# Kernel optimization log

Hardware: AMD Instinct MI355X
Metric: run time of the kernel (lower is better)

The kernel has to match this reference:

```python
import jax, jax.numpy as jnp
import numpy as np

K_ATTRS = 16  # fixed number of attribute clusters (torch.unique made static for jit)
NEG_INF = jnp.float32(-1e9)


def setup_inputs() -> dict:
    key = jax.random.key(0)
    ks = jax.random.split(key, 20)
    B, T, V, D, H = 4096, 200, 100000, 64, 64
    M0, M1 = 256, 128
    FC_IN = D + D + H + D  # 256
    s = 0.02
    f32 = jnp.float32
    inp = {
        "item_id": jax.random.randint(ks[0], (B,), 0, V),
        "hist_item_ids": jax.random.randint(ks[1], (B, T), 0, V),
        "hist_item_attributes": jax.random.randint(ks[2], (B, T), 0, K_ATTRS),
        "emb_table": s * jax.random.normal(ks[3], (V, D), dtype=f32),
        "au_W1": s * jax.random.normal(ks[4], (4 * D, H), dtype=f32),
        "au_b1": jnp.zeros((H,), f32),
        "au_W2": s * jax.random.normal(ks[5], (H, 1), dtype=f32),
        "au_b2": jnp.zeros((1,), f32),
        "gru_Wx": s * jax.random.normal(ks[6], (D, 3 * H), dtype=f32),
        "gru_Wh": s * jax.random.normal(ks[7], (H, 3 * H), dtype=f32),
        "gru_b": jnp.zeros((3 * H,), f32),
        "fc_W0": s * jax.random.normal(ks[8], (FC_IN, M0), dtype=f32),
        "fc_b0": jnp.zeros((M0,), f32),
        "fc_W1": s * jax.random.normal(ks[9], (M0, M1), dtype=f32),
        "fc_b1": jnp.zeros((M1,), f32),
        "final_W": s * jax.random.normal(ks[10], (M1, 1), dtype=f32),
        "final_b": jnp.zeros((1,), f32),
    }
    return inp


def reference(item_id, hist_item_ids, hist_item_attributes, emb_table,
              au_W1, au_b1, au_W2, au_b2, gru_Wx, gru_Wh, gru_b,
              fc_W0, fc_b0, fc_W1, fc_b1, final_W, final_b):
    item = emb_table[item_id]            # [B,D]
    hist = emb_table[hist_item_ids]      # [B,T,D]
    B = item.shape[0]
    H = gru_Wh.shape[0]

    # --- DIEN: GRU over history, final hidden state ---
    xp = hist @ gru_Wx + gru_b           # [B,T,3H]

    def step(h, x):
        gz, gr, gn = jnp.split(h @ gru_Wh, 3, axis=-1)
        xz, xr, xn = jnp.split(x, 3, axis=-1)
        z = jax.nn.sigmoid(xz + gz)
        r = jax.nn.sigmoid(xr + gr)
        n = jnp.tanh(xn + r * gn)
        return (1.0 - z) * n + z * h, None

    h0 = jnp.zeros((B, H), hist.dtype)
    interest_evolution, _ = jax.lax.scan(step, h0, jnp.swapaxes(xp, 0, 1))  # [B,H]

    # --- DIN-style activation unit: score each key against the target item ---
    def act_unit(q, keys):  # q:[B,D], keys:[B,N,D] -> [B,N,1]
        qe = jnp.broadcast_to(q[:, None, :], keys.shape)
        feat = jnp.concatenate([keys, qe, keys - qe, keys * qe], axis=-1)
        hid = jax.nn.relu(feat @ au_W1 + au_b1)
        return hid @ au_W2 + au_b2

    w1 = act_unit(item, hist)                    # [B,T,1]
    user_interest_l1 = jnp.sum(w1 * hist, axis=1)  # [B,D]

    # --- attribute_group: per-attribute masked softmax + weighted sum ---
    mask = hist_item_attributes[..., None] == jnp.arange(K_ATTRS)  # [B,T,K]
    logits = jnp.where(mask, w1, NEG_INF)        # [B,T,K]
    probs = jax.nn.softmax(logits, axis=1) * mask
    cluster = jnp.einsum('btk,btd->bkd', probs, hist)  # [B,K,D]

    w2 = act_unit(item, cluster)                 # [B,K,1]
    user_interest_l2 = jnp.sum(w2 * cluster, axis=1)  # [B,D]

    combined = jnp.concatenate(
        [user_interest_l1, user_interest_l2, interest_evolution, item], axis=1)
    x = jax.nn.relu(combined @ fc_W0 + fc_b0)
    x = jax.nn.relu(x @ fc_W1 + fc_b1)
    out = x @ final_W + final_b                  # [B,1]
    return jax.nn.sigmoid(out[:, 0])             # [B]
```

## Files before the change

kernel.cpp:

```cpp
#include <hip/hip_runtime.h>
#include <hip/hip_bf16.h>

#define B_   4096
#define T_   200
#define KA   16

#define OFF_BG  0
#define OFF_WQ  4096
#define OFF_QP  (OFF_BG  + B_*T_)
#define OFF_UI1 (OFF_QP  + B_*64)
#define OFF_UI2 (OFF_UI1 + B_*64)
#define OFF_HF  (OFF_UI2 + B_*64)
#define OFF_CL  (OFF_HF  + B_*64)

typedef __attribute__((ext_vector_type(8))) short bf16x8;
typedef __attribute__((ext_vector_type(4))) float f32x4;

__device__ __forceinline__ float sigmoidf_(float x) {
  return 1.f / (1.f + __expf(-x));
}
__device__ __forceinline__ float sigf(float x) {
  return __builtin_amdgcn_rcpf(1.f + __builtin_amdgcn_exp2f(-1.44269504f * x));
}
__device__ __forceinline__ float tanhfast(float y) {
  return 1.f - 2.f * __builtin_amdgcn_rcpf(1.f + __builtin_amdgcn_exp2f(2.88539008f * y));
}
__device__ __forceinline__ short f2bf(float x) {
  unsigned u = __float_as_uint(x);
  unsigned r = (u + 0x7fffu + ((u >> 16) & 1u)) >> 16;
  return (short)r;
}
__device__ __forceinline__ unsigned cvtpk(float lo, float hi) {
  unsigned r;
  asm("v_cvt_pk_bf16_f32 %0, %1, %2" : "=v"(r) : "v"(lo), "v"(hi));
  return r;
}
union BF8 { bf16x8 v; unsigned u[4]; };

__device__ __forceinline__ bf16x8 pack8(float4 f0, float4 f1) {
  BF8 a;
  a.u[0] = cvtpk(f0.x, f0.y);
  a.u[1] = cvtpk(f0.z, f0.w);
  a.u[2] = cvtpk(f1.x, f1.y);
  a.u[3] = cvtpk(f1.z, f1.w);
  return a.v;
}
__device__ __forceinline__ bf16x8 pack8m(float4 f0, float4 f1,
                                         float4 q0, float4 q1) {
  BF8 a;
  a.u[0] = cvtpk(f0.x*q0.x, f0.y*q0.y);
  a.u[1] = cvtpk(f0.z*q0.z, f0.w*q0.w);
  a.u[2] = cvtpk(f1.x*q1.x, f1.y*q1.y);
  a.u[3] = cvtpk(f1.z*q1.z, f1.w*q1.w);
  return a.v;
}


__global__ __launch_bounds__(256) void k_prep(
    const float* __restrict__ auW1, short* __restrict__ bg,
    float* __restrict__ wq)
{
  const int i = blockIdx.x*256 + threadIdx.x;
  if (i < 8192) {
    const int k = i >> 6, col = i & 63;
    float v;
    if (k < 64) v = auW1[k*64 + col] + auW1[2*4096 + k*64 + col];
    else        v = auW1[3*4096 + (k-64)*64 + col];
    bg[((k >> 5)*4 + ((k >> 3) & 3))*512 + col*8 + (k & 7)] = f2bf(v);
  } else if (i < 12288) {
    const int j = i - 8192;
    wq[j] = auW1[(64 + (j >> 6))*64 + (j & 63)]
          - auW1[(128 + (j >> 6))*64 + (j & 63)];
  }
}

__global__ __launch_bounds__(256) void k_act1(
    const int* __restrict__ item_id, const int* __restrict__ hist_ids,
    const int* __restrict__ attrs,
    const float* __restrict__ emb, const float* __restrict__ aub1,
    const float* __restrict__ auW2, const float* __restrict__ aub2,
    const short* __restrict__ bg_in, const float* __restrict__ wq_in,
    float* __restrict__ qp_out, float* __restrict__ ui1_out,
    float* __restrict__ cluster_out)
{
  __shared__ __align__(16) char sPool[16384];
  __shared__ float sW1[208];
  __shared__ float sP[200];
  __shared__ float sM[KA], sE[KA];
  __shared__ float sItem[64], sQp[64];
  __shared__ float sQpP[4][64];
  __shared__ float sUi[4][64];
  __shared__ int   sIds[200], sAttr[200];

  short* sB2 = (short*)sPool;
  float (*sAcc)[KA][64] = (float (*)[KA][64])sPool;

  const int b = blockIdx.x;
  const int tid = threadIdx.x;
  const int wave = tid >> 6, lane = tid & 63;
  const int g = lane >> 4;
  const int c15 = lane & 15;
  const int itrow = item_id[b];

  for (int i = tid; i < 4096; i += 256)
    ((unsigned*)sB2)[i] = ((const unsigned*)bg_in)[i];
  if (tid < 64) sItem[tid] = emb[(size_t)itrow*64 + tid];
  if (tid < T_) {
    sIds[tid]  = hist_ids[(size_t)b*T_ + tid];
    sAttr[tid] = attrs[(size_t)b*T_ + tid];
  }
  __syncthreads();

  {
    const int j = tid & 63, iq = tid >> 6;
    float acc = 0.f;
    #pragma unroll
    for (int ii = 0; ii < 16; ++ii) {
      const int i = iq*16 + ii;
      acc += sItem[i] * wq_in[i*64 + j];
    }
    sQpP[iq][j] = acc;
  }
  __syncthreads();
  if (tid < 64) {
    float q = aub1[tid] + sQpP[0][tid] + sQpP[1][tid] + sQpP[2][tid] + sQpP[3][tid];
    sQp[tid] = q;
    qp_out[(size_t)b*64 + tid] = q;
  }
  __syncthreads();

  const float4* itemp = (const float4*)(emb + (size_t)itrow*64);
  float4 q0 = itemp[g*2],     q1 = itemp[g*2 + 1];
  float4 q2 = itemp[8 + g*2], q3 = itemp[8 + g*2 + 1];

  bf16x8 bfr[4][4];
  #pragma unroll
  for (int kk = 0; kk < 4; ++kk) {
    #pragma unroll
    for (int n = 0; n < 4; ++n)
      bfr[kk][n] = *(const bf16x8*)&sB2[(kk*4 + g)*512 + (n*16 + c15)*8];
  }
  float w2v[4], qpv[4];
  #pragma unroll
  for (int n = 0; n < 4; ++n) {
    w2v[n] = auW2[n*16 + c15];
    qpv[n] = sQp[n*16 + c15];
  }
  const float b2v = aub2[0];
  __syncthreads();

  for (int i = tid; i < 4*KA*64; i += 256) ((float*)sAcc)[i] = 0.f;

  {
    float4 c0, c1, c2, c3;
    {
      const int t = wave*16 + c15;
      const int tc = (t < T_) ? t : (T_ - 1);
      const float4* kp = (const float4*)(emb + (size_t)sIds[tc]*64);
      c0 = kp[g*2];     c1 = kp[g*2 + 1];
      c2 = kp[8 + g*2]; c3 = kp[8 + g*2 + 1];
    }
    for (int tt = wave; tt < 13; tt += 4) {
      float4 n0{0,0,0,0}, n1{0,0,0,0}, n2{0,0,0,0}, n3{0,0,0,0};
      const int ttn = tt + 4;
      if (ttn < 13) {
        const int t = ttn*16 + c15;
        const int tc = (t < T_) ? t : (T_ - 1);
        const float4* kp = (const float4*)(emb + (size_t)sIds[tc]*64);
        n0 = kp[g*2];     n1 = kp[g*2 + 1];
        n2 = kp[8 + g*2]; n3 = kp[8 + g*2 + 1];
      }

      bf16x8 a0 = pack8(c0, c1);
      bf16x8 a1 = pack8(c2, c3);
      bf16x8 a2 = pack8m(c0, c1, q0, q1);
      bf16x8 a3 = pack8m(c2, c3, q2, q3);

      f32x4 acc[4];
      #pragma unroll
      for (int n = 0; n < 4; ++n) acc[n] = f32x4{qpv[n], qpv[n], qpv[n], qpv[n]};
      #pragma unroll
      for (int n = 0; n < 4; ++n) {
        acc[n] = __builtin_amdgcn_mfma_f32_16x16x32_bf16(a0, bfr[0][n], acc[n], 0, 0, 0);
        acc[n] = __builtin_amdgcn_mfma_f32_16x16x32_bf16(a1, bfr[1][n], acc[n], 0, 0, 0);
        acc[n] = __builtin_amdgcn_mfma_f32_16x16x32_bf16(a2, bfr[2][n], acc[n], 0, 0, 0);
        acc[n] = __builtin_amdgcn_mfma_f32_16x16x32_bf16(a3, bfr[3][n], acc[n], 0, 0, 0);
      }
      float ws[4] = {0.f, 0.f, 0.f, 0.f};
      #pragma unroll
      for (int n = 0; n < 4; ++n) {
        #pragma unroll
        for (int r = 0; r < 4; ++r)
          ws[r] += fmaxf(acc[n][r], 0.f) * w2v[n];
      }
      #pragma unroll
      for (int r = 0; r < 4; ++r) {
        ws[r] += __shfl_xor(ws[r], 1);
        ws[r] += __shfl_xor(ws[r], 2);
        ws[r] += __shfl_xor(ws[r], 4);
        ws[r] += __shfl_xor(ws[r], 8);
        ws[r] += b2v;
      }
      if (c15 == 0) {
        #pragma unroll
        for (int r = 0; r < 4; ++r) {
          const int trow = tt*16 + g*4 + r;
          if (trow < T_) sW1[trow] = ws[r];
        }
      }
      c0 = n0; c1 = n1; c2 = n2; c3 = n3;
    }
  }
  __syncthreads();

  for (int k = wave; k < KA; k += 4) {
    float m = -1e9f;
    for (int tt4 = 0; tt4 < 4; ++tt4) {
      int t = tt4*64 + lane;
      if (t < T_ && sAttr[t] == k) m = fmaxf(m, sW1[t]);
    }
    #pragma unroll
    for (int off = 32; off > 0; off >>= 1) m = fmaxf(m, __shfl_xor(m, off));
    float e = 0.f;
    for (int tt4 = 0; tt4 < 4; ++tt4) {
      int t = tt4*64 + lane;
      if (t < T_ && sAttr[t] == k) e += __expf(sW1[t] - m);
    }
    #pragma unroll
    for (int off = 32; off > 0; off >>= 1) e += __shfl_xor(e, off);
    if (lane == 0) { sM[k] = m; sE[k] = e; }
  }
  __syncthreads();
  if (tid < T_) {
    int k = sAttr[tid];
    float e = sE[k];
    sP[tid] = (e > 0.f) ? __expf(sW1[tid] - sM[k]) * __builtin_amdgcn_rcpf(e) : 0.f;
  }
  __syncthreads();

  {
    float uiacc = 0.f;
    #define LDV(tt) (((tt) < T_) ? emb[(size_t)sIds[tt]*64 + lane] : 0.f)
    float v0 = LDV(wave), v1 = LDV(wave + 4), v2 = LDV(wave + 8), v3 = LDV(wave + 12);
    for (int t = wave; t < T_; t += 16) {
      float n0 = LDV(t + 16), n1 = LDV(t + 20), n2 = LDV(t + 24), n3 = LDV(t + 28);
      {
        const int tt = t;
        if (tt < T_) { sAcc[wave][sAttr[tt]][lane] += sP[tt] * v0; uiacc += sW1[tt] * v0; }
      }
      {
        const int tt = t + 4;
        if (tt < T_) { sAcc[wave][sAttr[tt]][lane] += sP[tt] * v1; uiacc += sW1[tt] * v1; }
      }
      {
        const int tt = t + 8;
        if (tt < T_) { sAcc[wave][sAttr[tt]][lane] += sP[tt] * v2; uiacc += sW1[tt] * v2; }
      }
      {
        const int tt = t + 12;
        if (tt < T_) { sAcc[wave][sAttr[tt]][lane] += sP[tt] * v3; uiacc += sW1[tt] * v3; }
      }
      v0 = n0; v1 = n1; v2 = n2; v3 = n3;
    }
    #undef LDV
    sUi[wave][lane] = uiacc;
  }
  __syncthreads();

  for (int i = tid; i < KA*64; i += 256) {
    cluster_out[(size_t)b*(KA*64) + i] =
        sAcc[0][0][i] + sAcc[1][0][i] + sAcc[2][0][i] + sAcc[3][0][i];
  }
  if (tid < 64) {
    ui1_out[(size_t)b*64 + tid] =
        sUi[0][tid] + sUi[1][tid] + sUi[2][tid] + sUi[3][tid];
  }
}

#define GRU_ROWS 16
__global__ __launch_bounds__(512) void k_gru(
    const int* __restrict__ hist_ids, const float* __restrict__ emb,
    const float* __restrict__ Wx, const float* __restrict__ Wh,
    const float* __restrict__ gb, float* __restrict__ hfin_out)
{
  __shared__ short sH[2][16*64];
  __shared__ short sX[4][16*64];
  __shared__ int   sIds[16*200];

  const int tid  = threadIdx.x;
  const int w    = tid >> 6;
  const int lane = tid & 63;
  const int g    = lane >> 4;
  const int c15  = lane & 15;
  const int b0   = blockIdx.x * GRU_ROWS;

  for (int i = tid; i < 16*200; i += 512) {
    const int r = i / 200, t = i - r*200;
    sIds[i] = hist_ids[(size_t)(b0 + r)*T_ + t];
  }
  for (int i = tid; i < 16*64; i += 512) sH[0][i] = 0;
  __syncthreads();

  if (w >= 4) {
    const int stane = (w - 4)*64 + lane;
    const int srow  = stane >> 4;
    const int scol  = (stane & 15) * 4;
    const int sidx  = srow*64 + (((scol >> 3) ^ (srow & 7))*8) + (scol & 7);
    const int* idrow = &sIds[srow*200];
    #pragma unroll
    for (int p = 0; p < 2; ++p) {
      const float4 f = *(const float4*)(emb + (size_t)idrow[p]*64 + scol);
      uint2 u; u.x = cvtpk(f.x, f.y); u.y = cvtpk(f.z, f.w);
      *(uint2*)&sX[p][sidx] = u;
    }
    __syncthreads();
    for (int t = 0; t < T_; ++t) {
      const int t2 = (t + 2 < T_) ? (t + 2) : (T_ - 1);
      const float4 f = *(const float4*)(emb + (size_t)idrow[t2]*64 + scol);
      uint2 u; u.x = cvtpk(f.x, f.y); u.y = cvtpk(f.z, f.w);
      *(uint2*)&sX[(t + 2) & 3][sidx] = u;
      __syncthreads();
    }
  } else {
    bf16x8 bx[3][2], bh[3][2];
    #pragma unroll
    for (int l = 0; l < 3; ++l) {
      const int jb = (l*4 + w)*16 + c15;
      #pragma unroll
      for (int kk = 0; kk < 2; ++kk) {
        bf16x8 vx, vh;
        #pragma unroll
        for (int e = 0; e < 8; ++e) {
          const int krow = kk*32 + g*8 + e;
          vx[e] = f2bf(Wx[(size_t)krow*192 + jb]);
          vh[e] = f2bf(Wh[(size_t)krow*192 + jb]);
        }
        bx[l][kk] = vx; bh[l][kk] = vh;
      }
    }
    float bias[3];
    #pragma unroll
    for (int l = 0; l < 3; ++l) bias[l] = gb[l*64 + w*16 + c15];

    const int rs = c15 & 7;
    const int ridx0 = c15*64 + ((g    ) ^ rs)*8;
    const int ridx1 = c15*64 + ((g + 4) ^ rs)*8;
    int widx[4];
    {
      const int unit = w*2 + (c15 >> 3);
      #pragma unroll
      for (int r = 0; r < 4; ++r) {
        const int row = g*4 + r;
        widx[r] = row*64 + ((unit ^ (row & 7))*8) + (c15 & 7);
      }
    }
    float hold[4] = {0.f, 0.f, 0.f, 0.f};
    __syncthreads();

    #pragma unroll 2
    for (int t = 0; t < T_; ++t) {
      const short* hbuf = sH[t & 1];
      short*       hnxt = sH[(t & 1) ^ 1];
      const short* xbuf = sX[t & 3];

      bf16x8 ax0 = *(const bf16x8*)&xbuf[ridx0];
      bf16x8 ax1 = *(const bf16x8*)&xbuf[ridx1];
      bf16x8 ah0 = *(const bf16x8*)&hbuf[ridx0];
      bf16x8 ah1 = *(const bf16x8*)&hbuf[ridx1];

      f32x4 aX[3], aH[3];
      #pragma unroll
      for (int l = 0; l < 3; ++l) {
        aX[l] = f32x4{bias[l], bias[l], bias[l], bias[l]};
        aH[l] = f32x4{0.f, 0.f, 0.f, 0.f};
      }
      #pragma unroll
      for (int l = 0; l < 3; ++l) {
        aH[l] = __builtin_amdgcn_mfma_f32_16x16x32_bf16(ah0, bh[l][0], aH[l], 0, 0, 0);
        aH[l] = __builtin_amdgcn_mfma_f32_16x16x32_bf16(ah1, bh[l][1], aH[l], 0, 0, 0);
        aX[l] = __builtin_amdgcn_mfma_f32_16x16x32_bf16(ax0, bx[l][0], aX[l], 0, 0, 0);
        aX[l] = __builtin_amdgcn_mfma_f32_16x16x32_bf16(ax1, bx[l][1], aX[l], 0, 0, 0);
      }

      #pragma unroll
      for (int r = 0; r < 4; ++r) {
        float z  = sigf(aX[0][r] + aH[0][r]);
        float rr = sigf(aX[1][r] + aH[1][r]);
        float nn = tanhfast(aX[2][r] + rr * aH[2][r]);
        hold[r] = nn + z * (hold[r] - nn);
        hnxt[widx[r]] = f2bf(hold[r]);
      }
      __syncthreads();
    }

    #pragma unroll
    for (int r = 0; r < 4; ++r)
      hfin_out[(size_t)(b0 + g*4 + r)*64 + w*16 + c15] = hold[r];
  }
}

__global__ __launch_bounds__(256) void k_act2(
    const int* __restrict__ item_id, const float* __restrict__ emb,
    const float* __restrict__ auW2, const float* __restrict__ aub2,
    const float* __restrict__ qp_in, const float* __restrict__ cluster_in,
    const short* __restrict__ bg_in, float* __restrict__ ui2_out)
{
  __shared__ short sB2[8192];
  __shared__ float sWs[4][16];
  __shared__ float sWf[16];
  __shared__ float sUi[4][64];

  const int b = blockIdx.x;
  const int tid = threadIdx.x;
  const int wave = tid >> 6, lane = tid & 63;
  const int g = lane >> 4;
  const int c15 = lane & 15;
  const int itrow = item_id[b];

  for (int i = tid; i < 4096; i += 256)
    ((unsigned*)sB2)[i] = ((const unsigned*)bg_in)[i];
  __syncthreads();

  const float4* itemp = (const float4*)(emb + (size_t)itrow*64);
  float4 q0 = itemp[g*2],     q1 = itemp[g*2 + 1];
  float4 q2 = itemp[8 + g*2], q3 = itemp[8 + g*2 + 1];
  const float4* kp = (const float4*)(cluster_in + (size_t)b*(KA*64) + c15*64);
  float4 k0 = kp[g*2],     k1 = kp[g*2 + 1];
  float4 k2 = kp[8 + g*2], k3 = kp[8 + g*2 + 1];
  bf16x8 a0 = pack8(k0, k1);
  bf16x8 a1 = pack8(k2, k3);
  bf16x8 a2 = pack8m(k0, k1, q0, q1);
  bf16x8 a3 = pack8m(k2, k3, q2, q3);

  const float qpv = qp_in[(size_t)b*64 + wave*16 + c15];
  const float w2v = auW2[wave*16 + c15];
  f32x4 acc = f32x4{qpv, qpv, qpv, qpv};
  acc = __builtin_amdgcn_mfma_f32_16x16x32_bf16(a0, *(const bf16x8*)&sB2[(0*4+g)*512 + (wave*16+c15)*8], acc, 0, 0, 0);
  acc = __builtin_amdgcn_mfma_f32_16x16x32_bf16(a1, *(const bf16x8*)&sB2[(1*4+g)*512 + (wave*16+c15)*8], acc, 0, 0, 0);
  acc = __builtin_amdgcn_mfma_f32_16x16x32_bf16(a2, *(const bf16x8*)&sB2[(2*4+g)*512 + (wave*16+c15)*8], acc, 0, 0, 0);
  acc = __builtin_amdgcn_mfma_f32_16x16x32_bf16(a3, *(const bf16x8*)&sB2[(3*4+g)*512 + (wave*16+c15)*8], acc, 0, 0, 0);

  float ws[4];
  #pragma unroll
  for (int r = 0; r < 4; ++r) {
    float v = fmaxf(acc[r], 0.f) * w2v;
    v += __shfl_xor(v, 1);
    v += __shfl_xor(v, 2);
    v += __shfl_xor(v, 4);
    v += __shfl_xor(v, 8);
    ws[r] = v;
  }
  if (c15 == 0) {
    #pragma unroll
    for (int r = 0; r < 4; ++r) sWs[wave][g*4 + r] = ws[r];
  }
  __syncthreads();
  if (tid < KA)
    sWf[tid] = sWs[0][tid] + sWs[1][tid] + sWs[2][tid] + sWs[3][tid] + aub2[0];
  __syncthreads();

  float uiacc = 0.f;
  #pragma unroll
  for (int kk = 0; kk < 4; ++kk) {
    const int k = wave*4 + kk;
    uiacc += sWf[k] * cluster_in[(size_t)b*(KA*64) + k*64 + lane];
  }
  sUi[wave][lane] = uiacc;
  __syncthreads();
  if (tid < 64) {
    ui2_out[(size_t)b*64 + tid] =
        sUi[0][tid] + sUi[1][tid] + sUi[2][tid] + sUi[3][tid];
  }
}

#define MLP_ROWS 16
__global__ __launch_bounds__(256) void k_mlp(
    const int* __restrict__ item_id, const float* __restrict__ emb,
    const float* __restrict__ ui1, const float* __restrict__ ui2,
    const float* __restrict__ hfin,
    const float* __restrict__ W0, const float* __restrict__ b0,
    const float* __restrict__ W1, const float* __restrict__ b1,
    const float* __restrict__ fW, const float* __restrict__ fb,
    float* __restrict__ out)
{
  __shared__ float sC[MLP_ROWS][256];
  __shared__ float sX0[MLP_ROWS][256];
  __shared__ float sX1[MLP_ROWS][128];
  const int tid = threadIdx.x;
  const int rb  = blockIdx.x * MLP_ROWS;

  for (int idx = tid; idx < MLP_ROWS*256; idx += 256) {
    int r = idx >> 8, c = idx & 255;
    size_t row = (size_t)(rb + r);
    float v;
    if (c < 64)       v = ui1[row*64 + c];
    else if (c < 128) v = ui2[row*64 + (c-64)];
    else if (c < 192) v = hfin[row*64 + (c-128)];
    else              v = emb[(size_t)item_id[row]*64 + (c-192)];
    sC[r][c] = v;
  }
  __syncthreads();
  {
    float acc[MLP_ROWS];
    #pragma unroll
    for (int r = 0; r < MLP_ROWS; ++r) acc[r] = b0[tid];
    #pragma unroll 4
    for (int i = 0; i < 256; ++i) {
      float w = W0[(size_t)i*256 + tid];
      #pragma unroll
      for (int r = 0; r < MLP_ROWS; ++r) acc[r] += sC[r][i] * w;
    }
    #pragma unroll
    for (int r = 0; r < MLP_ROWS; ++r) sX0[r][tid] = fmaxf(acc[r], 0.f);
  }
  __syncthreads();
  if (tid < 128) {
    float acc[MLP_ROWS];
    #pragma unroll
    for (int r = 0; r < MLP_ROWS; ++r) acc[r] = b1[tid];
    #pragma unroll 4
    for (int i = 0; i < 256; ++i) {
      float w = W1[(size_t)i*128 + tid];
      #pragma unroll
      for (int r = 0; r < MLP_ROWS; ++r) acc[r] += sX0[r][i] * w;
    }
    #pragma unroll
    for (int r = 0; r < MLP_ROWS; ++r) sX1[r][tid] = fmaxf(acc[r], 0.f);
  }
  __syncthreads();
  {
    int r = tid >> 4, l16 = tid & 15;
    float p = 0.f;
    for (int i = l16; i < 128; i += 16) p += sX1[r][i] * fW[i];
    #pragma unroll
    for (int off = 8; off > 0; off >>= 1) p += __shfl_xor(p, off);
    if (l16 == 0) {
      float logit = p + fb[0];
      out[rb + r] = sigmoidf_(logit);
    }
  }
}

extern "C" void kernel_launch(void* const* d_in, const int* in_sizes, int n_in,
                              void* d_out, int out_size, void* d_ws, size_t ws_size,
                              hipStream_t stream)
{
  const int*   item_id  = (const int*)d_in[0];
  const int*   hist_ids = (const int*)d_in[1];
  const int*   attrs    = (const int*)d_in[2];
  const float* emb      = (const float*)d_in[3];
  const float* auW1     = (const float*)d_in[4];
  const float* aub1     = (const float*)d_in[5];
  const float* auW2     = (const float*)d_in[6];
  const float* aub2     = (const float*)d_in[7];
  const float* gWx      = (const float*)d_in[8];
  const float* gWh      = (const float*)d_in[9];
  const float* gb       = (const float*)d_in[10];
  const float* W0       = (const float*)d_in[11];
  const float* b0       = (const float*)d_in[12];
  const float* W1       = (const float*)d_in[13];
  const float* b1       = (const float*)d_in[14];
  const float* fW       = (const float*)d_in[15];
  const float* fb       = (const float*)d_in[16];

  float* out = (float*)d_out;
  float* ws  = (float*)d_ws;
  short* bg      = (short*)(ws + OFF_BG);
  float* wq      = ws + OFF_WQ;
  float* qp      = ws + OFF_QP;
  float* ui1     = ws + OFF_UI1;
  float* ui2     = ws + OFF_UI2;
  float* hfin    = ws + OFF_HF;
  float* cluster = ws + OFF_CL;

  k_prep<<<48, 256, 0, stream>>>(auW1, bg, wq);
  k_act1<<<B_, 256, 0, stream>>>(item_id, hist_ids, attrs, emb, aub1,
                                 auW2, aub2, bg, wq, qp, ui1, cluster);
  k_gru<<<B_/GRU_ROWS, 512, 0, stream>>>(hist_ids, emb, gWx, gWh, gb, hfin);
  k_act2<<<B_, 256, 0, stream>>>(item_id, emb, auW2, aub2, qp, cluster, bg,
                                 ui2);
  k_mlp<<<B_/MLP_ROWS, 256, 0, stream>>>(item_id, emb, ui1, ui2, hfin,
                                         W0, b0, W1, b1, fW, fb, out);
}
```

Before: 330.6 us.

## Fuse second activation unit into first kernel, keeping cluster vectors in LDS

The per-attribute cluster sums are now kept in shared memory inside k_act1. The second activation-unit MFMA scoring and weighted sum are computed in the same block, and the separate k_act2 launch is removed. This avoids writing and re-reading the 16×64 cluster tensor per row through global memory, and also saves one launch and one reload of the packed weights. The history gather loop is also simplified from a four-deep unrolled prefetch to a one-ahead prefetch. That may expose more gather latency, and the fused kernel uses more shared memory and registers, which could reduce occupancy.

```diff
diff --git a/kernel.cpp b/kernel.cpp
--- a/kernel.cpp
+++ b/kernel.cpp
@@ -81,15 +81,17 @@
     const float* __restrict__ auW2, const float* __restrict__ aub2,
     const short* __restrict__ bg_in, const float* __restrict__ wq_in,
     float* __restrict__ qp_out, float* __restrict__ ui1_out,
-    float* __restrict__ cluster_out)
+    float* __restrict__ ui2_out)
 {
   __shared__ __align__(16) char sPool[16384];
+  __shared__ __align__(16) float sCl[16][72];
   __shared__ float sW1[208];
   __shared__ float sP[200];
   __shared__ float sM[KA], sE[KA];
   __shared__ float sItem[64], sQp[64];
   __shared__ float sQpP[4][64];
   __shared__ float sUi[4][64];
+  __shared__ float sWf[16];
   __shared__ int   sIds[200], sAttr[200];
 
   short* sB2 = (short*)sPool;
@@ -240,39 +242,83 @@
 
   {
     float uiacc = 0.f;
-    #define LDV(tt) (((tt) < T_) ? emb[(size_t)sIds[tt]*64 + lane] : 0.f)
-    float v0 = LDV(wave), v1 = LDV(wave + 4), v2 = LDV(wave + 8), v3 = LDV(wave + 12);
-    for (int t = wave; t < T_; t += 16) {
-      float n0 = LDV(t + 16), n1 = LDV(t + 20), n2 = LDV(t + 24), n3 = LDV(t + 28);
-      {
-        const int tt = t;
-        if (tt < T_) { sAcc[wave][sAttr[tt]][lane] += sP[tt] * v0; uiacc += sW1[tt] * v0; }
-      }
-      {
-        const int tt = t + 4;
-        if (tt < T_) { sAcc[wave][sAttr[tt]][lane] += sP[tt] * v1; uiacc += sW1[tt] * v1; }
-      }
-      {
-        const int tt = t + 8;
-        if (tt < T_) { sAcc[wave][sAttr[tt]][lane] += sP[tt] * v2; uiacc += sW1[tt] * v2; }
-      }
-      {
-        const int tt = t + 12;
-        if (tt < T_) { sAcc[wave][sAttr[tt]][lane] += sP[tt] * v3; uiacc += sW1[tt] * v3; }
-      }
-      v0 = n0; v1 = n1; v2 = n2; v3 = n3;
-    }
-    #undef LDV
+    float vcur = emb[(size_t)sIds[wave]*64 + lane];
+    for (int t = wave; t < T_; t += 4) {
+      const int tn = t + 4;
+      float vnext = 0.f;
+      if (tn < T_) vnext = emb[(size_t)sIds[tn]*64 + lane];
+      const int k = sAttr[t];
+      sAcc[wave][k][lane] += sP[t] * vcur;
+      uiacc += sW1[t] * vcur;
+      vcur = vnext;
+    }
     sUi[wave][lane] = uiacc;
   }
   __syncthreads();
 
   for (int i = tid; i < KA*64; i += 256) {
-    cluster_out[(size_t)b*(KA*64) + i] =
-        sAcc[0][0][i] + sAcc[1][0][i] + sAcc[2][0][i] + sAcc[3][0][i];
+    const int k = i >> 6, f = i & 63;
+    sCl[k][f] = sAcc[0][0][i] + sAcc[1][0][i] + sAcc[2][0][i] + sAcc[3][0][i];
   }
   if (tid < 64) {
     ui1_out[(size_t)b*64 + tid] =
+        sUi[0][tid] + sUi[1][tid] + sUi[2][tid] + sUi[3][tid];
+  }
+  __syncthreads();
+
+  {
+    float4 cl0 = *(const float4*)&sCl[c15][g*8];
+    float4 cl1 = *(const float4*)&sCl[c15][g*8 + 4];
+    float4 cl2 = *(const float4*)&sCl[c15][32 + g*8];
+    float4 cl3 = *(const float4*)&sCl[c15][32 + g*8 + 4];
+    bf16x8 a0 = pack8(cl0, cl1);
+    bf16x8 a1 = pack8(cl2, cl3);
+    bf16x8 a2 = pack8m(cl0, cl1, q0, q1);
+    bf16x8 a3 = pack8m(cl2, cl3, q2, q3);
+
+    f32x4 acc[4];
+    #pragma unroll
+    for (int n = 0; n < 4; ++n) acc[n] = f32x4{qpv[n], qpv[n], qpv[n], qpv[n]};
+    #pragma unroll
+    for (int n = 0; n < 4; ++n) {
+      acc[n] = __builtin_amdgcn_mfma_f32_16x16x32_bf16(a0, bfr[0][n], acc[n], 0, 0, 0);
+      acc[n] = __builtin_amdgcn_mfma_f32_16x16x32_bf16(a1, bfr[1][n], acc[n], 0, 0, 0);
+      acc[n] = __builtin_amdgcn_mfma_f32_16x16x32_bf16(a2, bfr[2][n], acc[n], 0, 0, 0);
+      acc[n] = __builtin_amdgcn_mfma_f32_16x16x32_bf16(a3, bfr[3][n], acc[n], 0, 0, 0);
+    }
+    float ws[4] = {0.f, 0.f, 0.f, 0.f};
+    #pragma unroll
+    for (int n = 0; n < 4; ++n) {
+      #pragma unroll
+      for (int r = 0; r < 4; ++r)
+        ws[r] += fmaxf(acc[n][r], 0.f) * w2v[n];
+    }
+    #pragma unroll
+    for (int r = 0; r < 4; ++r) {
+      ws[r] += __shfl_xor(ws[r], 1);
+      ws[r] += __shfl_xor(ws[r], 2);
+      ws[r] += __shfl_xor(ws[r], 4);
+      ws[r] += __shfl_xor(ws[r], 8);
+    }
+    if (wave == 0 && c15 == 0) {
+      #pragma unroll
+      for (int r = 0; r < 4; ++r) sWf[g*4 + r] = ws[r] + b2v;
+    }
+  }
+  __syncthreads();
+
+  {
+    float uiacc = 0.f;
+    #pragma unroll
+    for (int kk = 0; kk < 4; ++kk) {
+      const int k = wave*4 + kk;
+      uiacc += sWf[k] * sCl[k][lane];
+    }
+    sUi[wave][lane] = uiacc;
+  }
+  __syncthreads();
+  if (tid < 64) {
+    ui2_out[(size_t)b*64 + tid] =
         sUi[0][tid] + sUi[1][tid] + sUi[2][tid] + sUi[3][tid];
   }
 }
@@ -396,80 +442,6 @@
     #pragma unroll
     for (int r = 0; r < 4; ++r)
       hfin_out[(size_t)(b0 + g*4 + r)*64 + w*16 + c15] = hold[r];
-  }
-}
-
-__global__ __launch_bounds__(256) void k_act2(
-    const int* __restrict__ item_id, const float* __restrict__ emb,
-    const float* __restrict__ auW2, const float* __restrict__ aub2,
-    const float* __restrict__ qp_in, const float* __restrict__ cluster_in,
-    const short* __restrict__ bg_in, float* __restrict__ ui2_out)
-{
-  __shared__ short sB2[8192];
-  __shared__ float sWs[4][16];
-  __shared__ float sWf[16];
-  __shared__ float sUi[4][64];
-
-  const int b = blockIdx.x;
-  const int tid = threadIdx.x;
-  const int wave = tid >> 6, lane = tid & 63;
-  const int g = lane >> 4;
-  const int c15 = lane & 15;
-  const int itrow = item_id[b];
-
-  for (int i = tid; i < 4096; i += 256)
-    ((unsigned*)sB2)[i] = ((const unsigned*)bg_in)[i];
-  __syncthreads();
-
-  const float4* itemp = (const float4*)(emb + (size_t)itrow*64);
-  float4 q0 = itemp[g*2],     q1 = itemp[g*2 + 1];
-  float4 q2 = itemp[8 + g*2], q3 = itemp[8 + g*2 + 1];
-  const float4* kp = (const float4*)(cluster_in + (size_t)b*(KA*64) + c15*64);
-  float4 k0 = kp[g*2],     k1 = kp[g*2 + 1];
-  float4 k2 = kp[8 + g*2], k3 = kp[8 + g*2 + 1];
-  bf16x8 a0 = pack8(k0, k1);
-  bf16x8 a1 = pack8(k2, k3);
-  bf16x8 a2 = pack8m(k0, k1, q0, q1);
-  bf16x8 a3 = pack8m(k2, k3, q2, q3);
-
-  const float qpv = qp_in[(size_t)b*64 + wave*16 + c15];
-  const float w2v = auW2[wave*16 + c15];
-  f32x4 acc = f32x4{qpv, qpv, qpv, qpv};
-  acc = __builtin_amdgcn_mfma_f32_16x16x32_bf16(a0, *(const bf16x8*)&sB2[(0*4+g)*512 + (wave*16+c15)*8], acc, 0, 0, 0);
-  acc = __builtin_amdgcn_mfma_f32_16x16x32_bf16(a1, *(const bf16x8*)&sB2[(1*4+g)*512 + (wave*16+c15)*8], acc, 0, 0, 0);
-  acc = __builtin_amdgcn_mfma_f32_16x16x32_bf16(a2, *(const bf16x8*)&sB2[(2*4+g)*512 + (wave*16+c15)*8], acc, 0, 0, 0);
-  acc = __builtin_amdgcn_mfma_f32_16x16x32_bf16(a3, *(const bf16x8*)&sB2[(3*4+g)*512 + (wave*16+c15)*8], acc, 0, 0, 0);
-
-  float ws[4];
-  #pragma unroll
-  for (int r = 0; r < 4; ++r) {
-    float v = fmaxf(acc[r], 0.f) * w2v;
-    v += __shfl_xor(v, 1);
-    v += __shfl_xor(v, 2);
-    v += __shfl_xor(v, 4);
-    v += __shfl_xor(v, 8);
-    ws[r] = v;
-  }
-  if (c15 == 0) {
-    #pragma unroll
-    for (int r = 0; r < 4; ++r) sWs[wave][g*4 + r] = ws[r];
-  }
-  __syncthreads();
-  if (tid < KA)
-    sWf[tid] = sWs[0][tid] + sWs[1][tid] + sWs[2][tid] + sWs[3][tid] + aub2[0];
-  __syncthreads();
-
-  float uiacc = 0.f;
-  #pragma unroll
-  for (int kk = 0; kk < 4; ++kk) {
-    const int k = wave*4 + kk;
-    uiacc += sWf[k] * cluster_in[(size_t)b*(KA*64) + k*64 + lane];
-  }
-  sUi[wave][lane] = uiacc;
-  __syncthreads();
-  if (tid < 64) {
-    ui2_out[(size_t)b*64 + tid] =
-        sUi[0][tid] + sUi[1][tid] + sUi[2][tid] + sUi[3][tid];
   }
 }
 
@@ -571,14 +543,11 @@
   float* ui1     = ws + OFF_UI1;
   float* ui2     = ws + OFF_UI2;
   float* hfin    = ws + OFF_HF;
-  float* cluster = ws + OFF_CL;
 
   k_prep<<<48, 256, 0, stream>>>(auW1, bg, wq);
   k_act1<<<B_, 256, 0, stream>>>(item_id, hist_ids, attrs, emb, aub1,
-                                 auW2, aub2, bg, wq, qp, ui1, cluster);
+                                 auW2, aub2, bg, wq, qp, ui1, ui2);
   k_gru<<<B_/GRU_ROWS, 512, 0, stream>>>(hist_ids, emb, gWx, gWh, gb, hfin);
-  k_act2<<<B_, 256, 0, stream>>>(item_id, emb, auW2, aub2, qp, cluster, bg,
-                                 ui2);
   k_mlp<<<B_/MLP_ROWS, 256, 0, stream>>>(item_id, emb, ui1, ui2, hfin,
                                          W0, b0, W1, b1, fW, fb, out);
 }
```

After: 342.1 us. 3.5% more time.
